# Performance work log

Hardware: AMD Instinct MI355X
Metric: run time of the kernel (lower is better)

Reference implementation:

```python
import jax, jax.numpy as jnp
import numpy as np

FIRING_THRESHOLD = 1.0
EPS = 1e-4
E_MAX = 2  # static upper bound on extra multi-firing steps (scaled weights < 1 here)


def _cif(inputs, input_weights, padding_mask, target_lengths, Tmax):
    """Training-mode CIF (target_lengths provided). Faithful to torch module,
    except cumsum in float32 (torch uses float64) and the durations run-length
    encoding is vectorized instead of a per-sample python loop."""
    B, S, C = inputs.shape
    w = jnp.clip(input_weights, 0.0, 1.0)
    w = jnp.where(padding_mask, 0.0, w)
    w_sum = w.sum(-1)  # input_weights_sum (pre-scaling)
    desired = FIRING_THRESHOLD * target_lengths.astype(inputs.dtype) + EPS
    w = w * (desired / w_sum)[:, None]  # scaled alpha
    csum = jnp.cumsum(w, axis=-1)  # (B,S); torch uses float64 here
    right_idx = jnp.clip(jnp.floor(csum / FIRING_THRESHOLD).astype(jnp.int32), 0, Tmax)
    left_idx = jnp.concatenate([jnp.zeros((B, 1), jnp.int32), right_idx[:, :-1]], axis=1)
    n_fir = right_idx - left_idx
    extra = jnp.maximum(n_fir - 1, 0)
    bI = jnp.arange(B)[:, None]
    src_range = jnp.arange(1, S + 1, dtype=inputs.dtype)[None, :]
    right_w = jnp.where(n_fir > 0, csum - right_idx.astype(csum.dtype) * FIRING_THRESHOLD, 0.0).astype(inputs.dtype)
    left_w = (w - right_w - extra.astype(w.dtype) * FIRING_THRESHOLD).astype(inputs.dtype)
    output = jnp.zeros((B, Tmax + 1, C), inputs.dtype)
    delay = jnp.zeros((B, Tmax + 1), inputs.dtype)
    output = output.at[bI, right_idx].add(right_w[..., None] * inputs)
    delay = delay.at[bI, right_idx].add(right_w * src_range / FIRING_THRESHOLD)
    output = output.at[bI, left_idx].add(left_w[..., None] * inputs)
    delay = delay.at[bI, left_idx].add(left_w * src_range / FIRING_THRESHOLD)
    # multi-firing extra scatter steps, static bound + masking (torch: python loop over extra_steps)
    src_feats = inputs * FIRING_THRESHOLD
    tgt = left_idx
    for k in range(1, E_MAX + 1):
        tgt = jnp.minimum(tgt + 1, Tmax)
        mk = (extra >= k)
        output = output.at[bI, tgt].add(src_feats * mk[..., None])
        delay = delay.at[bI, tgt].add(src_range * mk)
    output = output[:, :Tmax]
    delay = delay[:, :Tmax]
    # durations: run-length encoding of rounded cumsum (vectorized; torch loops per sample)
    padded_idx = jnp.round(csum).astype(jnp.int32)  # nondecreasing
    tl = target_lengths.astype(jnp.int32)[:, None]
    seq = jnp.minimum(jnp.concatenate([padded_idx, tl], axis=1), tl)  # (B,S+1): prefix < tl kept, rest clamped to tl
    chg = (seq[:, 1:] != seq[:, :-1]).astype(jnp.int32)
    run_id = jnp.concatenate([jnp.zeros((B, 1), jnp.int32), jnp.cumsum(chg, axis=1)], axis=1)  # (B,S+1)
    m = run_id[:, -1]  # number of non-final runs per sample
    flat_ids = (jnp.arange(B)[:, None] * (Tmax + 1) + run_id).reshape(-1)
    counts = jax.ops.segment_sum(jnp.ones(B * (S + 1), jnp.int32), flat_ids, num_segments=B * (Tmax + 1)).reshape(B, Tmax + 1)
    r = jnp.arange(Tmax + 1)[None, :]
    dur = jnp.where(r < m[:, None], counts, 0)  # drop final (tail) run, zero-pad
    L = jnp.where(m >= target_lengths.astype(jnp.int32), m, m + 1)  # torch pads one zero if short
    audio_len = (~padding_mask).sum(-1).astype(jnp.int32)
    dur = dur.at[jnp.arange(B), L - 1].add(audio_len - dur.sum(-1))
    dur = dur[:, :Tmax]
    return output, delay, dur, w_sum, right_w, left_w


def setup_inputs():
    key = jax.random.key(0)
    k1, k2 = jax.random.split(key)
    B, S, C, Tmax = 32, 2048, 512, 512
    inputs = jax.random.normal(k1, (B, S, C), dtype=jnp.float32)
    input_weights = jax.random.uniform(k2, (B, S), dtype=jnp.float32)
    padding_mask = jnp.zeros((B, S), dtype=bool)
    target_lengths = jnp.full((B,), Tmax, dtype=jnp.int32)
    return {"inputs": inputs, "input_weights": input_weights, "padding_mask": padding_mask,
            "target_lengths": target_lengths, "Tmax": Tmax}


def reference(inputs, input_weights, padding_mask, target_lengths, Tmax):
    return _cif(inputs, input_weights, padding_mask, target_lengths, Tmax)
```

## Files before the change

### kernel.cpp

```cpp
#include <hip/hip_runtime.h>

#define FT 1.0f

__device__ __forceinline__ int seqv_at(const int* pad, int S, int tl, int j) {
  return (j < S) ? min(pad[j], tl) : tl;
}

__device__ __forceinline__ int lower_b(const int* pad, int S, int tl, int v) {
  int lo = 0, hi = S + 1;
  while (lo < hi) { int mid = (lo + hi) >> 1; if (seqv_at(pad, S, tl, mid) >= v) hi = mid; else lo = mid + 1; }
  return lo;
}
__device__ __forceinline__ int upper_b(const int* pad, int S, int tl, int v) {
  int lo = 0, hi = S + 1;
  while (lo < hi) { int mid = (lo + hi) >> 1; if (seqv_at(pad, S, tl, mid) > v) hi = mid; else lo = mid + 1; }
  return lo;
}

__global__ __launch_bounds__(1024) void cif_row_kernel(
    const float* __restrict__ iw, const unsigned char* __restrict__ mask,
    const int* __restrict__ tlen,
    float* __restrict__ o_wsum, float* __restrict__ o_rw, float* __restrict__ o_lw,
    float* __restrict__ o_delay, float* __restrict__ o_dur,
    int* __restrict__ a_ws, int S, int T)
{
  extern __shared__ float smem[];
  float* w     = smem;
  float* lv    = smem + S;
  float* rwArr = smem + 2 * S;
  int*   pad   = (int*)(smem + 3 * S);
  float* red   = smem + 4 * S;
  int*   aa    = (int*)(smem + 4 * S + 64);
  __shared__ int s_alen, s_m;

  const int b = blockIdx.x, tid = threadIdx.x, nt = blockDim.x;
  const float* iwr = iw + (size_t)b * S;
  const unsigned char* mr = mask + (size_t)b * S;
  const int tl = tlen[b];

  if (tid == 0) { s_alen = 0; s_m = 0; }
  __syncthreads();

  int myal = 0;
  for (int s = tid; s < S; s += nt) {
    float v = iwr[s];
    v = fminf(fmaxf(v, 0.0f), 1.0f);
    if (mr[s]) v = 0.0f; else myal++;
    w[s] = v;
  }
  atomicAdd(&s_alen, myal);
  __syncthreads();

  if (tid < 16) {
    float acc = 0.0f;
    for (int i = tid; i < S; i += 16) acc += w[i];
    red[tid] = acc;
  }
  __syncthreads();
  for (int h = 8; h >= 1; h >>= 1) {
    if (tid < h) red[tid] = red[tid] + red[tid + h];
    __syncthreads();
  }
  const float wsum = red[0];
  if (tid == 0) o_wsum[b] = wsum;

  const float desired = FT * (float)tl + 1e-4f;
  const float scale = desired / wsum;
  for (int s = tid; s < S; s += nt) { float sv = w[s] * scale; w[s] = sv; lv[s] = sv; }
  for (int i = tid; i <= T; i += nt) aa[i] = (i == 0) ? -1 : S;
  __syncthreads();

  {
    int offp = 0, off = S, sz = S >> 1;
    while (sz >= 1) {
      for (int i = tid; i < sz; i += nt)
        lv[off + i] = lv[offp + 2 * i] + lv[offp + 2 * i + 1];
      __syncthreads();
      offp = off; off += sz; sz >>= 1;
    }
  }
  {
    int K = 0; while ((1 << K) < S) K++;
    for (int k = K - 1; k >= 0; --k) {
      int szk = S >> k;
      int ok  = 2 * S - 2 * szk;
      int ok1 = 2 * S - szk;
      for (int j = tid; j < szk; j += nt) {
        if (j == 0) continue;
        if (j & 1) lv[ok + j] = lv[ok1 + (j >> 1)];
        else       lv[ok + j] = lv[ok1 + (j >> 1) - 1] + lv[ok + j];
      }
      __syncthreads();
    }
  }

  for (int s = tid; s < S; s += nt) {
    float c = lv[s];
    int ri = (int)floorf(c / FT); ri = min(max(ri, 0), T);
    int li = 0;
    if (s > 0) { int rp = (int)floorf(lv[s - 1] / FT); li = min(max(rp, 0), T); }
    int n = ri - li;
    int ex = max(n - 1, 0);
    float rw = (n > 0) ? (c - (float)ri * FT) : 0.0f;
    float lwv = (w[s] - rw) - (float)ex * FT;
    o_rw[(size_t)b * S + s] = rw;
    o_lw[(size_t)b * S + s] = lwv;
    rwArr[s] = rw;
    pad[s] = (int)rintf(c);
    if (n > 0) aa[ri] = s;
  }
  __syncthreads();

  {
    int my = 0;
    for (int j = tid; j < S; j += nt)
      my += (seqv_at(pad, S, tl, j) != seqv_at(pad, S, tl, j + 1));
    atomicAdd(&s_m, my);
  }
  __syncthreads();
  const int m = s_m;
  const int alen = s_alen;
  const int seq0 = seqv_at(pad, S, tl, 0);
  const int L = (m >= tl) ? m : m + 1;

  for (int t = tid; t < T; t += nt) {
    int start = aa[t], end = aa[t + 1];
    int s0 = (start < 0) ? 0 : start;
    int s1 = min(end, S - 1);
    float d = 0.0f;
    for (int s = s0; s <= s1; ++s) {
      float cf = (s == start) ? rwArr[s] : (w[s] - rwArr[s]);
      d = d + (cf * (float)(s + 1)) / FT;
    }
    o_delay[(size_t)b * T + t] = d;
  }

  for (int t = tid; t < T; t += nt) {
    int dv = 0;
    if (t < m) {
      int v = seq0 + t;
      dv = upper_b(pad, S, tl, v) - lower_b(pad, S, tl, v);
    }
    if (t == L - 1) dv += alen - lower_b(pad, S, tl, tl);
    o_dur[(size_t)b * T + t] = (float)dv;
  }
}

__global__ void cif_gather_kernel(const float* __restrict__ in,
    const float* __restrict__ rw, const float* __restrict__ lw,
    const int* __restrict__ a_ws, float* __restrict__ out,
    int S, int T, int C)
{
  const int t = blockIdx.x, b = blockIdx.y;
  const int* ab = a_ws + (size_t)b * (T + 1);
  const int start = ab[t];
  const int end = ab[t + 1];
  const int s0 = (start < 0) ? 0 : start;
  const int s1 = min(end, S - 1);
  const size_t bS = (size_t)b * S;
  const int c4 = threadIdx.x * 4;
  float4 acc = make_float4(0.f, 0.f, 0.f, 0.f);
  for (int s = s0; s <= s1; ++s) {
    const float coeff = (s == start) ? rw[bS + s] : lw[bS + s];
    const float4 v = *reinterpret_cast<const float4*>(in + (bS + s) * (size_t)C + c4);
    acc.x += coeff * v.x; acc.y += coeff * v.y;
    acc.z += coeff * v.z; acc.w += coeff * v.w;
  }
  *reinterpret_cast<float4*>(out + ((size_t)b * T + t) * (size_t)C + c4) = acc;
}

extern "C" void kernel_launch(void* const* d_in, const int* in_sizes, int n_in,
                              void* d_out, int out_size, void* d_ws, size_t ws_size,
                              hipStream_t stream)
{
  const float* inp = (const float*)d_in[0];
  const float* iw  = (const float*)d_in[1];
  const unsigned char* mask = (const unsigned char*)d_in[2];
  const int* tl = (const int*)d_in[3];
  const int B = in_sizes[3];
  const int S = in_sizes[1] / B;
  const int C = in_sizes[0] / in_sizes[1];
  const long long T = ((long long)out_size - B - 2LL * B * S) / ((long long)B * C + 2LL * B);

  float* o = (float*)d_out;
  float* o_out   = o;
  float* o_delay = o_out + (size_t)B * T * C;
  float* o_dur   = o_delay + (size_t)B * T;
  float* o_wsum  = o_dur + (size_t)B * T;
  float* o_rw    = o_wsum + B;
  float* o_lw    = o_rw + (size_t)B * S;
  int* a_ws = (int*)d_ws;

  size_t smem = (size_t)(4 * S + 64) * sizeof(float) + (size_t)(T + 1) * sizeof(int);
  hipLaunchKernelGGL(cif_row_kernel, dim3(B), dim3(1024), smem, stream,
                     iw, mask, tl, o_wsum, o_rw, o_lw, o_delay, o_dur, a_ws, S, (int)T);
  dim3 g2((unsigned)T, (unsigned)B);
  hipLaunchKernelGGL(cif_gather_kernel, g2, dim3(C / 4), 0, stream,
                     inp, o_rw, o_lw, a_ws, o_out, S, (int)T, C);
}
```

Before: 35.75 us.

## Use wave-level barriers for small scan levels and batch bins in gather

The row kernel drops to 512 threads. Its final reduction steps and the small upper levels of the Blelloch scan now run inside a single 64-lane wavefront with wave barriers instead of block-wide __syncthreads. The gather kernel processes four output bins per block and loads their boundaries once, cutting block count and per-block setup. This trades some parallelism in the row kernel and depends on wavefront-synchronous shared-memory behaviour for correctness.

```diff
diff --git a/kernel.cpp b/kernel.cpp
--- a/kernel.cpp
+++ b/kernel.cpp
@@ -17,7 +17,7 @@
   return lo;
 }
 
-__global__ __launch_bounds__(1024) void cif_row_kernel(
+__global__ __launch_bounds__(512) void cif_row_kernel(
     const float* __restrict__ iw, const unsigned char* __restrict__ mask,
     const int* __restrict__ tlen,
     float* __restrict__ o_wsum, float* __restrict__ o_rw, float* __restrict__ o_lw,
@@ -56,11 +56,15 @@
     for (int i = tid; i < S; i += 16) acc += w[i];
     red[tid] = acc;
   }
-  __syncthreads();
-  for (int h = 8; h >= 1; h >>= 1) {
-    if (tid < h) red[tid] = red[tid] + red[tid + h];
-    __syncthreads();
-  }
+  __builtin_amdgcn_wave_barrier();
+  if (tid < 8) red[tid] = red[tid] + red[tid + 8];
+  __builtin_amdgcn_wave_barrier();
+  if (tid < 4) red[tid] = red[tid] + red[tid + 4];
+  __builtin_amdgcn_wave_barrier();
+  if (tid < 2) red[tid] = red[tid] + red[tid + 2];
+  __builtin_amdgcn_wave_barrier();
+  if (tid == 0) red[0] = red[0] + red[1];
+  __syncthreads();
   const float wsum = red[0];
   if (tid == 0) o_wsum[b] = wsum;
 
@@ -70,18 +74,36 @@
   for (int i = tid; i <= T; i += nt) aa[i] = (i == 0) ? -1 : S;
   __syncthreads();
 
+  int K = 0; while ((1 << K) < S) K++;
+
   {
     int offp = 0, off = S, sz = S >> 1;
-    while (sz >= 1) {
+    while (sz >= 64) {
       for (int i = tid; i < sz; i += nt)
         lv[off + i] = lv[offp + 2 * i] + lv[offp + 2 * i + 1];
       __syncthreads();
       offp = off; off += sz; sz >>= 1;
     }
-  }
-  {
-    int K = 0; while ((1 << K) < S) K++;
-    for (int k = K - 1; k >= 0; --k) {
+    if (tid < 64) {
+      while (sz >= 1) {
+        if (tid < sz)
+          lv[off + tid] = lv[offp + 2 * tid] + lv[offp + 2 * tid + 1];
+        __builtin_amdgcn_wave_barrier();
+        offp = off; off += sz; sz >>= 1;
+      }
+      for (int k = K - 1; k >= K - 6; --k) {
+        int szk = S >> k;
+        int ok  = 2 * S - 2 * szk;
+        int ok1 = 2 * S - szk;
+        if (tid > 0 && tid < szk) {
+          if (tid & 1) lv[ok + tid] = lv[ok1 + (tid >> 1)];
+          else         lv[ok + tid] = lv[ok1 + (tid >> 1) - 1] + lv[ok + tid];
+        }
+        __builtin_amdgcn_wave_barrier();
+      }
+    }
+    __syncthreads();
+    for (int k = K - 7; k >= 0; --k) {
       int szk = S >> k;
       int ok  = 2 * S - 2 * szk;
       int ok1 = 2 * S - szk;
@@ -146,27 +168,37 @@
   }
 }
 
-__global__ void cif_gather_kernel(const float* __restrict__ in,
+#define KBINS 4
+__global__ __launch_bounds__(128) void cif_gather_kernel(const float* __restrict__ in,
     const float* __restrict__ rw, const float* __restrict__ lw,
     const int* __restrict__ a_ws, float* __restrict__ out,
     int S, int T, int C)
 {
-  const int t = blockIdx.x, b = blockIdx.y;
+  const int b = blockIdx.y;
+  const int t0 = blockIdx.x * KBINS;
   const int* ab = a_ws + (size_t)b * (T + 1);
-  const int start = ab[t];
-  const int end = ab[t + 1];
-  const int s0 = (start < 0) ? 0 : start;
-  const int s1 = min(end, S - 1);
   const size_t bS = (size_t)b * S;
   const int c4 = threadIdx.x * 4;
-  float4 acc = make_float4(0.f, 0.f, 0.f, 0.f);
-  for (int s = s0; s <= s1; ++s) {
-    const float coeff = (s == start) ? rw[bS + s] : lw[bS + s];
-    const float4 v = *reinterpret_cast<const float4*>(in + (bS + s) * (size_t)C + c4);
-    acc.x += coeff * v.x; acc.y += coeff * v.y;
-    acc.z += coeff * v.z; acc.w += coeff * v.w;
-  }
-  *reinterpret_cast<float4*>(out + ((size_t)b * T + t) * (size_t)C + c4) = acc;
+
+  int bound[KBINS + 1];
+#pragma unroll
+  for (int k = 0; k <= KBINS; ++k) bound[k] = ab[min(t0 + k, T)];
+
+#pragma unroll
+  for (int k = 0; k < KBINS; ++k) {
+    const int t = t0 + k;
+    if (t >= T) break;
+    const int st = bound[k];
+    const int en = min(bound[k + 1], S - 1);
+    float4 acc = make_float4(0.f, 0.f, 0.f, 0.f);
+    for (int s = (st < 0 ? 0 : st); s <= en; ++s) {
+      const float coeff = (s == st) ? rw[bS + s] : lw[bS + s];
+      const float4 v = *reinterpret_cast<const float4*>(in + (bS + s) * (size_t)C + c4);
+      acc.x += coeff * v.x; acc.y += coeff * v.y;
+      acc.z += coeff * v.z; acc.w += coeff * v.w;
+    }
+    *reinterpret_cast<float4*>(out + ((size_t)b * T + t) * (size_t)C + c4) = acc;
+  }
 }
 
 extern "C" void kernel_launch(void* const* d_in, const int* in_sizes, int n_in,
@@ -192,9 +224,9 @@
   int* a_ws = (int*)d_ws;
 
   size_t smem = (size_t)(4 * S + 64) * sizeof(float) + (size_t)(T + 1) * sizeof(int);
-  hipLaunchKernelGGL(cif_row_kernel, dim3(B), dim3(1024), smem, stream,
+  hipLaunchKernelGGL(cif_row_kernel, dim3(B), dim3(512), smem, stream,
                      iw, mask, tl, o_wsum, o_rw, o_lw, o_delay, o_dur, a_ws, S, (int)T);
-  dim3 g2((unsigned)T, (unsigned)B);
+  dim3 g2((unsigned)((T + KBINS - 1) / KBINS), (unsigned)B);
   hipLaunchKernelGGL(cif_gather_kernel, g2, dim3(C / 4), 0, stream,
                      inp, o_rw, o_lw, a_ws, o_out, S, (int)T, C);
 }
```

Measured after the change: 32.71 us. 1.09x faster.
